# Performance work log

Measured on AMD Instinct MI355X. Metric: run time of the kernel, lower is better.

The kernel has to match this reference:

```python
import jax, jax.numpy as jnp
import numpy as np
import math

IN_CH = 512
KEY_SIZE = 512
VALUE_SIZE = 512
B, T = 8, 2048


def setup_inputs() -> dict:
    key = jax.random.key(0)
    ks = jax.random.split(key, 7)
    s = 1.0 / math.sqrt(IN_CH)
    return {
        "x": jax.random.normal(ks[0], (B, T, IN_CH), dtype=jnp.float32),
        "Wq": jax.random.uniform(ks[1], (IN_CH, KEY_SIZE), jnp.float32, -s, s),
        "bq": jax.random.uniform(ks[2], (KEY_SIZE,), jnp.float32, -s, s),
        "Wk": jax.random.uniform(ks[3], (IN_CH, KEY_SIZE), jnp.float32, -s, s),
        "bk": jax.random.uniform(ks[4], (KEY_SIZE,), jnp.float32, -s, s),
        "Wv": jax.random.uniform(ks[5], (IN_CH, VALUE_SIZE), jnp.float32, -s, s),
        "bv": jax.random.uniform(ks[6], (VALUE_SIZE,), jnp.float32, -s, s),
    }


def reference(x, Wq, bq, Wk, bk, Wv, bv):
    # Projections (single head)
    q = jnp.einsum('btc,ck->btk', x, Wq) + bq  # [B,T,K]
    k = jnp.einsum('btc,ck->btk', x, Wk) + bk  # [B,T,K]
    v = jnp.einsum('btc,cv->btv', x, Wv) + bv  # [B,T,V]
    # Full score matrix, causal mask (strictly upper triangle masked: col > row)
    scores = jnp.einsum('bqk,btk->bqt', q, k)  # [B,T,T]
    t = scores.shape[1]
    causal = jnp.arange(t)[None, :] > jnp.arange(t)[:, None]  # True where future
    scores = jnp.where(causal[None], -jnp.inf, scores)
    attn = jax.nn.softmax(scores / math.sqrt(KEY_SIZE), axis=2)
    out = jnp.einsum('bqt,btv->bqv', attn, v)  # [B,T,V]
    return jnp.concatenate((x, out), axis=2)  # [B,T,C+V]
```

## Files before the change

kernel.cpp:

```cpp
#include <hip/hip_runtime.h>


#define DEV __device__ __forceinline__

typedef unsigned short u16;
typedef unsigned int u32;
typedef __attribute__((ext_vector_type(8))) short short8;
typedef __attribute__((ext_vector_type(4))) float float4v;

DEV u16 f2bf(float f) {
    u32 u = __float_as_uint(f);
    return (u16)((u + 0x7FFFu + ((u >> 16) & 1u)) >> 16);
}
DEV float bf2f(u16 h) { return __uint_as_float(((u32)h) << 16); }

DEV float4v mfma16(short8 a, short8 b, float4v c) {
    return __builtin_amdgcn_mfma_f32_16x16x32_bf16(a, b, c, 0, 0, 0);
}

#define GLD16(gptr, lptr)                                                     \
    __builtin_amdgcn_global_load_lds(                                         \
        (const __attribute__((address_space(1))) void*)(gptr),                \
        (__attribute__((address_space(3))) void*)(lptr), 16, 0, 0)

__global__ void prep_k(const void* __restrict__ x,
                       const void* __restrict__ Wq, const void* __restrict__ Wk,
                       const void* __restrict__ Wv, const void* __restrict__ bq,
                       const void* __restrict__ bk, const void* __restrict__ bv,
                       int* __restrict__ flag, u16* __restrict__ xb,
                       void* __restrict__ out, u16* __restrict__ Wt,
                       u16* __restrict__ bbuf) {
    __shared__ __attribute__((aligned(16))) u16 T[64 * 80];
    int tid = threadIdx.x;
    int lane = tid & 63;
    u32 ws = ((const u32*)x)[lane * 16];
    int e = (ws >> 7) & 0xFF;
    unsigned long long m = __ballot(e >= 0x60 && e <= 0x90);
    int isbf = (__popcll(m) > 32) ? 1 : 0;

    int bid = blockIdx.x;
    if (bid == 0 && tid == 0) flag[0] = isbf;

    if (bid < 4096) {
        int i0 = (bid * 256 + tid) * 8;
        int row = i0 >> 9, col = i0 & 511;
        if (isbf) {
            uint4 v = *(const uint4*)((const u16*)x + i0);
            *(uint4*)&xb[i0] = v;
            *(uint4*)((u16*)out + (size_t)row * 1024 + col) = v;
        } else {
            const float* xf = (const float*)x;
            float4 f0 = *(const float4*)(xf + i0);
            float4 f1 = *(const float4*)(xf + i0 + 4);
            union { u16 us[8]; uint4 v; } pk;
            pk.us[0] = f2bf(f0.x); pk.us[1] = f2bf(f0.y);
            pk.us[2] = f2bf(f0.z); pk.us[3] = f2bf(f0.w);
            pk.us[4] = f2bf(f1.x); pk.us[5] = f2bf(f1.y);
            pk.us[6] = f2bf(f1.z); pk.us[7] = f2bf(f1.w);
            *(uint4*)&xb[i0] = pk.v;
            float* o = (float*)out + (size_t)row * 1024 + col;
            *(float4*)o = f0; *(float4*)(o + 4) = f1;
        }
        return;
    }

    if (bid >= 4288) {
        int j = bid - 4288;
        int z = j >> 1;
        int i = (j & 1) * 256 + tid;
        const void* s = (z == 0) ? bq : ((z == 1) ? bk : bv);
        bbuf[z * 512 + i] = isbf ? ((const u16*)s)[i]
                                 : f2bf(((const float*)s)[i]);
        return;
    }

    int widx = bid - 4096;
    int z = widx >> 6;
    int t64 = widx & 63;
    int k0 = (t64 >> 3) * 64, n0 = (t64 & 7) * 64;
    const void* W = (z == 0) ? Wq : ((z == 1) ? Wk : Wv);
    if (isbf) {
        #pragma unroll
        for (int p = 0; p < 2; p++) {
            int idx = p * 256 + tid;
            int k = idx >> 3, c8 = idx & 7;
            short8 v = *(const short8*)((const u16*)W + (size_t)(k0 + k) * 512 + n0 + c8 * 8);
            #pragma unroll
            for (int j = 0; j < 8; j++)
                T[(c8 * 8 + j) * 80 + k] = (u16)v[j];
        }
    } else {
        #pragma unroll
        for (int p = 0; p < 4; p++) {
            int idx = p * 256 + tid;
            int k = idx >> 4, c4 = idx & 15;
            float4 f = *(const float4*)((const float*)W + (size_t)(k0 + k) * 512 + n0 + c4 * 4);
            T[(c4 * 4 + 0) * 80 + k] = f2bf(f.x);
            T[(c4 * 4 + 1) * 80 + k] = f2bf(f.y);
            T[(c4 * 4 + 2) * 80 + k] = f2bf(f.z);
            T[(c4 * 4 + 3) * 80 + k] = f2bf(f.w);
        }
    }
    __syncthreads();
    #pragma unroll
    for (int p = 0; p < 2; p++) {
        int idx = p * 256 + tid;
        int n = idx >> 3, c8 = idx & 7;
        short8 o = *(const short8*)&T[n * 80 + c8 * 8];
        *(uint4*)&Wt[z * 262144 + (size_t)(n0 + n) * 512 + k0 + c8 * 8] = *(uint4*)&o;
    }
}

#define PWB(N)                                                                \
    do {                                                                      \
        asm volatile("s_waitcnt vmcnt(" #N ")" ::: "memory");                 \
        __builtin_amdgcn_s_barrier();                                         \
        asm volatile("" ::: "memory");                                        \
    } while (0)

__global__ __launch_bounds__(256) void proj_k(
        const u16* __restrict__ x, const u16* __restrict__ Wt,
        const u16* __restrict__ bb,
        u16* __restrict__ Qo, u16* __restrict__ Ko, u16* __restrict__ Vt_out) {
    int L = blockIdx.x;
    int xcd = L & 7;
    int t8 = L >> 3;
    int q8 = t8 / 12;
    int zn = t8 - q8 * 12;
    int mBase = (q8 * 8 + xcd) * 128;
    int z = zn >> 2;
    int nBase = (zn & 3) * 128;
    const u16* Wz = Wt + z * 262144;
    const u16* bias = bb + z * 512;

    __shared__ __attribute__((aligned(16))) u16 LDSBUF[16384];
#define XSB(bi) (&LDSBUF[(bi) * 4096])
#define WSB(bi) (&LDSBUF[8192 + (bi) * 4096])

    int tid = threadIdx.x;
    int w = tid >> 6, lane = tid & 63, quad = lane >> 4, l16 = lane & 15;
    int wr = (w >> 1) * 64, wc = (w & 1) * 64;

#define PISSUE(bi, k0)                                                        \
    { _Pragma("unroll")                                                       \
      for (int gg = 0; gg < 2; gg++) {                                        \
        int g = w * 2 + gg;                                                   \
        int row = g * 16 + (lane >> 2);                                       \
        int c8 = (lane & 3) ^ ((row >> 1) & 3);                               \
        GLD16(&x [(size_t)(mBase + row) * 512 + (k0) + c8 * 8], &XSB(bi)[g * 512]); \
        GLD16(&Wz[(size_t)(nBase + row) * 512 + (k0) + c8 * 8], &WSB(bi)[g * 512]); \
      } }

    PISSUE(0, 0)
    PISSUE(1, 32)

    float4v acc[4][4] = {};

    #pragma unroll 2
    for (int t = 0; t < 16; t++) {
        int bi = t & 1;
        if (t < 15) { PWB(4); } else { PWB(0); }

        short8 a[4], b[4];
        #pragma unroll
        for (int mt = 0; mt < 4; mt++) {
            int rr = wr + mt * 16 + l16;
            a[mt] = *(const short8*)&XSB(bi)[rr * 32 + ((quad ^ ((rr >> 1) & 3)) * 8)];
        }
        #pragma unroll
        for (int nt = 0; nt < 4; nt++) {
            int rr = wc + nt * 16 + l16;
            b[nt] = *(const short8*)&WSB(bi)[rr * 32 + ((quad ^ ((rr >> 1) & 3)) * 8)];
        }
        #pragma unroll
        for (int mt = 0; mt < 4; mt++)
            #pragma unroll
            for (int nt = 0; nt < 4; nt++)
                acc[mt][nt] = mfma16(a[mt], b[nt], acc[mt][nt]);

        if (t < 14) {
            asm volatile("s_waitcnt lgkmcnt(0)" ::: "memory");
            __builtin_amdgcn_s_barrier();
            asm volatile("" ::: "memory");
            PISSUE(bi, (t + 2) * 32)
        }
    }

    __syncthreads();
    u16* stg = &LDSBUF[w * 4096];

    if (z == 2) {
        #pragma unroll
        for (int nt = 0; nt < 4; nt++) {
            int rl = nt * 16 + l16;
            float bval = bf2f(bias[nBase + wc + rl]);
            int rx = rl & 7;
            #pragma unroll
            for (int mt = 0; mt < 4; mt++) {
                int g  = mt * 2 + (quad >> 1);
                int b0 = (quad & 1) * 4;
                float4v v = acc[mt][nt];
                u16 t0 = f2bf(v[0] + bval), t1 = f2bf(v[1] + bval);
                u16 t2 = f2bf(v[2] + bval), t3 = f2bf(v[3] + bval);
                uint2 pk = make_uint2((u32)t0 | ((u32)t1 << 16),
                                      (u32)t2 | ((u32)t3 << 16));
                *(uint2*)&stg[rl * 64 + ((g ^ rx) << 3) + b0] = pk;
            }
        }
        asm volatile("s_waitcnt lgkmcnt(0)" ::: "memory");
        __syncthreads();
        int bbi = (mBase + wr) >> 11;
        int tt0 = (mBase + wr) & 2047;
        #pragma unroll
        for (int i = 0; i < 8; i++) {
            int rl = i * 8 + (lane >> 3);
            int c8 = lane & 7;
            short8 s = *(const short8*)&stg[rl * 64 + ((c8 ^ (rl & 7)) << 3)];
            *(uint4*)&Vt_out[((size_t)bbi * 512 + nBase + wc + rl) * 2048 +
                             tt0 + c8 * 8] = *(uint4*)&s;
        }
    } else {
        u16* dst = (z == 0) ? Qo : Ko;
        #pragma unroll
        for (int nt = 0; nt < 4; nt++) {
            int cl = nt * 16 + l16;
            float bval = bf2f(bias[nBase + wc + cl]);
            int g = nt * 2 + (l16 >> 3);
            int b = l16 & 7;
            #pragma unroll
            for (int mt = 0; mt < 4; mt++) {
                float4v v = acc[mt][nt];
                #pragma unroll
                for (int r = 0; r < 4; r++) {
                    int rl = mt * 16 + quad * 4 + r;
                    stg[rl * 64 + ((g ^ (rl & 7)) << 3) + b] = f2bf(v[r] + bval);
                }
            }
        }
        asm volatile("s_waitcnt lgkmcnt(0)" ::: "memory");
        __syncthreads();
        #pragma unroll
        for (int i = 0; i < 8; i++) {
            int rl = i * 8 + (lane >> 3);
            int c8 = lane & 7;
            short8 s = *(const short8*)&stg[rl * 64 + ((c8 ^ (rl & 7)) << 3)];
            *(uint4*)&dst[(size_t)(mBase + wr + rl) * 512 +
                          nBase + wc + c8 * 8] = *(uint4*)&s;
        }
    }
#undef PISSUE
#undef XSB
#undef WSB
}


#define LOADK(dst, kB, half)                                                  \
    { _Pragma("unroll")                                                       \
      for (int j = 0; j < 8; j++) {                                           \
        int row2 = 2 * (j * 4 + w);                                           \
        int row = row2 + (lane >> 5);                                         \
        int col8 = lane & 31;                                                 \
        GLD16(&Kb[(size_t)((kB) + row) * 512 + (half) * 256 +                 \
                  ((col8 ^ (row & 7)) << 3)], &dst[row2 * 256]);              \
      } }

#define LOADV(dst, kB, half)                                                  \
    { _Pragma("unroll")                                                       \
      for (int j = 0; j < 8; j++) {                                           \
        int blk8 = 8 * (j * 4 + w);                                           \
        int dl = blk8 + (lane >> 3);                                          \
        int col8 = lane & 7;                                                  \
        GLD16(&Vb[(size_t)((half) * 256 + dl) * 2048 + (kB) +                 \
                  ((col8 ^ (dl & 7)) << 3)], &dst[blk8 * 64]);                \
      } }

#define SSTEP(buf, h)                                                         \
    { _Pragma("unroll")                                                       \
      for (int kk = 0; kk < 8; kk++) {                                        \
        _Pragma("unroll")                                                     \
        for (int nt = 0; nt < 4; nt++) {                                      \
          short8 bf = *(const short8*)&buf[(nt * 16 + l16) * 256 +            \
                                           (((kk * 4 + quad) ^ sw) << 3)];    \
          accS[nt] = mfma16(qf[(h) * 8 + kk], bf, accS[nt]);                  \
        } } }

#define PVSTEP(buf, accO)                                                     \
    { _Pragma("unroll")                                                       \
      for (int kk = 0; kk < 2; kk++) {                                        \
        _Pragma("unroll")                                                     \
        for (int dt = 0; dt < 4; dt++) {                                      \
          int rowv = w * 64 + dt * 16 + l16;                                  \
          short8 bf = *(const short8*)&buf[rowv * 64 +                        \
                                           (((kk * 4 + quad) ^ sw) << 3)];    \
          _Pragma("unroll")                                                   \
          for (int mt = 0; mt < 4; mt++)                                      \
            accO[dt][mt] = mfma16(pf[mt][kk], bf, accO[dt][mt]);              \
        } } }

__global__ __launch_bounds__(256, 1) void attn_k(
        const u16* __restrict__ Q, const u16* __restrict__ K,
        const u16* __restrict__ Vt, const int* __restrict__ flag,
        void* __restrict__ out, u16* __restrict__ Opart,
        float2* __restrict__ ml, int dosplit) {
    int blk = blockIdx.x;
    int b, qt, h, kt0, kt1;
    if (dosplit) {
        qt = (blk < 256) ? (31 - (blk >> 4)) : ((blk - 256) >> 4);
        h  = (blk >> 3) & 1;
        b  = blk & 7;
        int n = qt + 1, mid = n >> 1;
        kt0 = h ? mid : 0;
        kt1 = h ? n : mid;
    } else {
        qt = 31 - (blk >> 3);
        h  = 0;
        b  = blk & 7;
        kt0 = 0; kt1 = qt + 1;
    }
    int q0 = qt * 64;
    int isbf = flag[0];

    __shared__ __attribute__((aligned(16))) u16 KV0[16384];
    __shared__ __attribute__((aligned(16))) u16 KV1[16384];
    __shared__ __attribute__((aligned(16))) u16 Ps[4096];
    __shared__ float al_s[64];
    __shared__ float il_s[64];
    __shared__ int skip_s[4];

    int tid = threadIdx.x;
    int w = tid >> 6, lane = tid & 63, quad = lane >> 4, l16 = lane & 15;
    int sw = l16 & 7;

    const u16* Qb = Q  + (size_t)b * 2048 * 512;
    const u16* Kb = K  + (size_t)b * 2048 * 512;
    const u16* Vb = Vt + (size_t)b * 512 * 2048;

    if (kt0 < kt1) LOADK(KV0, kt0 * 64, 0);

    short8 qf[16];
    {
        const u16* Qrow = &Qb[(size_t)(q0 + w * 16 + l16) * 512];
        #pragma unroll
        for (int g = 0; g < 16; g++)
            qf[g] = *(const short8*)&Qrow[g * 32 + quad * 8];
    }

    float4v accO0[4][4] = {};
    float4v accO1[4][4] = {};
    float4v accS[4] = {};
    short8 pf[4][2];
    float mrow[4] = {-1e30f, -1e30f, -1e30f, -1e30f};
    float lrow[4] = {0.f, 0.f, 0.f, 0.f};
    const float scale = 0.044194173824159216f;

    __syncthreads();

    for (int kt = kt0; kt < kt1; kt++) {
        int kB = kt * 64;

        LOADK(KV1, kB, 1);
        SSTEP(KV0, 0);
        __syncthreads();

        LOADV(KV0, kB, 0);
        SSTEP(KV1, 1);
        {
            int diag = (kt == qt);
            float pv[4][4], lmx[4], alpha[4];
            #pragma unroll
            for (int r = 0; r < 4; r++) {
                float mx = -1e30f;
                #pragma unroll
                for (int nt = 0; nt < 4; nt++) {
                    float sv = accS[nt][r] * scale;
                    if (diag && (nt * 16 + l16 > w * 16 + quad * 4 + r)) sv = -1e30f;
                    pv[nt][r] = sv;
                    mx = fmaxf(mx, sv);
                }
                lmx[r] = mx;
            }
            int small = (lmx[0] - mrow[0] <= 8.f) && (lmx[1] - mrow[1] <= 8.f) &&
                        (lmx[2] - mrow[2] <= 8.f) && (lmx[3] - mrow[3] <= 8.f);
            int wskip = __all(small) ? 1 : 0;
            if (lane == 0) skip_s[w] = wskip;
            if (wskip) {
                #pragma unroll
                for (int r = 0; r < 4; r++) alpha[r] = 1.0f;
            } else {
                #pragma unroll
                for (int r = 0; r < 4; r++) {
                    float mx = lmx[r];
                    mx = fmaxf(mx, __shfl_xor(mx, 1));
                    mx = fmaxf(mx, __shfl_xor(mx, 2));
                    mx = fmaxf(mx, __shfl_xor(mx, 4));
                    mx = fmaxf(mx, __shfl_xor(mx, 8));
                    float mnew = fmaxf(mrow[r], mx);
                    alpha[r] = __expf(mrow[r] - mnew);
                    mrow[r] = mnew;
                }
            }
            #pragma unroll
            for (int r = 0; r < 4; r++) {
                float sum = 0.f;
                #pragma unroll
                for (int nt = 0; nt < 4; nt++) {
                    pv[nt][r] = __expf(pv[nt][r] - mrow[r]);
                    sum += pv[nt][r];
                }
                lrow[r] = lrow[r] * alpha[r] + sum;
            }
            #pragma unroll
            for (int nt = 0; nt < 4; nt++)
                #pragma unroll
                for (int r = 0; r < 4; r++)
                    Ps[(w * 16 + quad * 4 + r) * 64 + nt * 16 + l16] = f2bf(pv[nt][r]);
            #pragma unroll
            for (int r = 0; r < 4; r++) al_s[w * 16 + quad * 4 + r] = alpha[r];
            #pragma unroll
            for (int nt = 0; nt < 4; nt++) accS[nt] = (float4v){0.f, 0.f, 0.f, 0.f};
        }
        __syncthreads();

        LOADV(KV1, kB, 1);
        {
            #pragma unroll
            for (int mt = 0; mt < 4; mt++)
                #pragma unroll
                for (int kk = 0; kk < 2; kk++)
                    pf[mt][kk] = *(const short8*)&Ps[(mt * 16 + l16) * 64 +
                                                     kk * 32 + quad * 8];
            int bskip = skip_s[0] & skip_s[1] & skip_s[2] & skip_s[3];
            if (!bskip) {
                float alf[4][4];
                #pragma unroll
                for (int mt = 0; mt < 4; mt++)
                    #pragma unroll
                    for (int r = 0; r < 4; r++)
                        alf[mt][r] = al_s[mt * 16 + quad * 4 + r];
                #pragma unroll
                for (int dt = 0; dt < 4; dt++)
                    #pragma unroll
                    for (int mt = 0; mt < 4; mt++)
                        #pragma unroll
                        for (int r = 0; r < 4; r++) {
                            accO0[dt][mt][r] *= alf[mt][r];
                            accO1[dt][mt][r] *= alf[mt][r];
                        }
            }
        }
        PVSTEP(KV0, accO0);
        __syncthreads();

        if (kt + 1 < kt1) LOADK(KV0, kB + 64, 0);
        PVSTEP(KV1, accO1);
        __syncthreads();
    }

    #pragma unroll
    for (int r = 0; r < 4; r++) {
        lrow[r] += __shfl_xor(lrow[r], 1);
        lrow[r] += __shfl_xor(lrow[r], 2);
        lrow[r] += __shfl_xor(lrow[r], 4);
        lrow[r] += __shfl_xor(lrow[r], 8);
    }

    if (dosplit) {
        if (l16 == 0) {
            #pragma unroll
            for (int r = 0; r < 4; r++) {
                int grow = b * 2048 + q0 + w * 16 + quad * 4 + r;
                ml[h * 16384 + grow] = make_float2(mrow[r], lrow[r]);
            }
        }
        #pragma unroll
        for (int dt = 0; dt < 4; dt++) {
            int dg = w * 64 + dt * 16 + l16;
            #pragma unroll
            for (int mt = 0; mt < 4; mt++)
                #pragma unroll
                for (int r = 0; r < 4; r++) {
                    int grow = b * 2048 + q0 + mt * 16 + quad * 4 + r;
                    size_t base = ((size_t)h * 16384 + grow) * 512;
                    Opart[base + dg]       = f2bf(accO0[dt][mt][r]);
                    Opart[base + dg + 256] = f2bf(accO1[dt][mt][r]);
                }
        }
    } else {
        #pragma unroll
        for (int r = 0; r < 4; r++) il_s[w * 16 + quad * 4 + r] = 1.0f / lrow[r];
        __syncthreads();
        float invl[4][4];
        #pragma unroll
        for (int mt = 0; mt < 4; mt++)
            #pragma unroll
            for (int r = 0; r < 4; r++) invl[mt][r] = il_s[mt * 16 + quad * 4 + r];
        u16*   o16 = (u16*)out;
        float* o32 = (float*)out;
        #pragma unroll
        for (int dt = 0; dt < 4; dt++) {
            int dg0 = 512 + w * 64 + dt * 16 + l16;
            #pragma unroll
            for (int mt = 0; mt < 4; mt++)
                #pragma unroll
                for (int r = 0; r < 4; r++) {
                    int rowg = q0 + mt * 16 + quad * 4 + r;
                    size_t base = ((size_t)b * 2048 + rowg) * 1024;
                    float v0 = accO0[dt][mt][r] * invl[mt][r];
                    float v1 = accO1[dt][mt][r] * invl[mt][r];
                    if (isbf) {
                        o16[base + dg0]       = f2bf(v0);
                        o16[base + dg0 + 256] = f2bf(v1);
                    } else {
                        o32[base + dg0]       = v0;
                        o32[base + dg0 + 256] = v1;
                    }
                }
        }
    }
}

__global__ __launch_bounds__(256) void combine_k(
        const u16* __restrict__ Opart, const float2* __restrict__ ml,
        const int* __restrict__ flag, void* __restrict__ out) {
    int tid = threadIdx.x;
    int grow = blockIdx.x * 4 + (tid >> 6);
    int d0 = (tid & 63) * 8;
    float2 ml0 = ml[grow], ml1 = ml[16384 + grow];
    float m = fmaxf(ml0.x, ml1.x);
    float a0 = __expf(ml0.x - m), a1 = __expf(ml1.x - m);
    float il = 1.0f / (ml0.y * a0 + ml1.y * a1);
    a0 *= il; a1 *= il;
    uint4 v0 = *(const uint4*)&Opart[(size_t)grow * 512 + d0];
    uint4 v1 = *(const uint4*)&Opart[(size_t)(16384 + grow) * 512 + d0];
    const u16* u0 = (const u16*)&v0;
    const u16* u1 = (const u16*)&v1;
    float res[8];
    #pragma unroll
    for (int i = 0; i < 8; i++)
        res[i] = bf2f(u0[i]) * a0 + bf2f(u1[i]) * a1;
    size_t base = (size_t)grow * 1024 + 512 + d0;
    if (flag[0]) {
        union { u16 us[8]; uint4 v; } pk;
        #pragma unroll
        for (int i = 0; i < 8; i++) pk.us[i] = f2bf(res[i]);
        *(uint4*)((u16*)out + base) = pk.v;
    } else {
        float* o = (float*)out + base;
        *(float4*)o = make_float4(res[0], res[1], res[2], res[3]);
        *(float4*)(o + 4) = make_float4(res[4], res[5], res[6], res[7]);
    }
}

extern "C" void kernel_launch(void* const* d_in, const int* in_sizes, int n_in,
                              void* d_out, int out_size, void* d_ws, size_t ws_size,
                              hipStream_t stream) {
    const void* x  = d_in[0];
    const void* Wq = d_in[1];
    const void* bq = d_in[2];
    const void* Wk = d_in[3];
    const void* bk = d_in[4];
    const void* Wv = d_in[5];
    const void* bv = d_in[6];

    u16* base = (u16*)d_ws;
    int* flag = (int*)base;
    u16* Wt   = base + 8;
    u16* bb   = Wt + 786432;
    u16* xb   = bb + 1544;
    u16* Qw   = xb + 8388608;
    u16* Kw   = Qw + 8388608;
    u16* Vtw  = Kw + 8388608;
    u16* Opart = Vtw + 8388608;
    float2* mlb = (float2*)(Opart + 16777216);

    size_t need = ((size_t)(Opart - base) + 16777216) * 2 + 262144;
    int dosplit = (ws_size >= need) ? 1 : 0;

    hipLaunchKernelGGL(prep_k, dim3(4294), dim3(256), 0, stream,
                       x, Wq, Wk, Wv, bq, bk, bv, flag, xb, d_out, Wt, bb);
    hipLaunchKernelGGL(proj_k, dim3(1536), dim3(256), 0, stream, xb, Wt, bb, Qw, Kw, Vtw);
    if (dosplit) {
        hipLaunchKernelGGL(attn_k, dim3(512), dim3(256), 0, stream,
                           Qw, Kw, Vtw, flag, d_out, Opart, mlb, 1);
        hipLaunchKernelGGL(combine_k, dim3(4096), dim3(256), 0, stream,
                           Opart, mlb, flag, d_out);
    } else {
        hipLaunchKernelGGL(attn_k, dim3(256), dim3(256), 0, stream,
                           Qw, Kw, Vtw, flag, d_out, Opart, mlb, 0);
    }
}
```

Before: 255.4 us.

## Fuse split-K combine into attention kernel via per-tile atomic counter

Removes the separate combine kernel. Each split attention block increments a per-(qtile,batch) counter after writing its partial output and softmax stats, and the second block to finish merges both halves and writes the final output. The counter is zeroed in the prep kernel. This saves a kernel launch and lets the merge overlap with other blocks' work, at the cost of threadfences, an atomic, and a serialized combine tail in the last-finishing block.

```diff
diff --git a/kernel.cpp b/kernel.cpp
--- a/kernel.cpp
+++ b/kernel.cpp
@@ -29,7 +29,7 @@
                        const void* __restrict__ bk, const void* __restrict__ bv,
                        int* __restrict__ flag, u16* __restrict__ xb,
                        void* __restrict__ out, u16* __restrict__ Wt,
-                       u16* __restrict__ bbuf) {
+                       u16* __restrict__ bbuf, int* __restrict__ cnt) {
     __shared__ __attribute__((aligned(16))) u16 T[64 * 80];
     int tid = threadIdx.x;
     int lane = tid & 63;
@@ -66,6 +66,7 @@
 
     if (bid >= 4288) {
         int j = bid - 4288;
+        if (j == 0) cnt[tid] = 0;
         int z = j >> 1;
         int i = (j & 1) * 256 + tid;
         const void* s = (z == 0) ? bq : ((z == 1) ? bk : bv);
@@ -301,7 +302,7 @@
         const u16* __restrict__ Q, const u16* __restrict__ K,
         const u16* __restrict__ Vt, const int* __restrict__ flag,
         void* __restrict__ out, u16* __restrict__ Opart,
-        float2* __restrict__ ml, int dosplit) {
+        float2* __restrict__ ml, int* __restrict__ cnt, int dosplit) {
     int blk = blockIdx.x;
     int b, qt, h, kt0, kt1;
     if (dosplit) {
@@ -326,6 +327,7 @@
     __shared__ float al_s[64];
     __shared__ float il_s[64];
     __shared__ int skip_s[4];
+    __shared__ int comb_s;
 
     int tid = threadIdx.x;
     int w = tid >> 6, lane = tid & 63, quad = lane >> 4, l16 = lane & 15;
@@ -484,6 +486,48 @@
                     Opart[base + dg]       = f2bf(accO0[dt][mt][r]);
                     Opart[base + dg + 256] = f2bf(accO1[dt][mt][r]);
                 }
+        }
+
+        __threadfence();
+        __syncthreads();
+        if (tid == 0) {
+            int old = atomicAdd(&cnt[qt * 8 + b], 1);
+            comb_s = (old == 1);
+        }
+        __syncthreads();
+        if (comb_s) {
+            __threadfence();
+            u16*   o16 = (u16*)out;
+            float* o32 = (float*)out;
+            #pragma unroll 4
+            for (int it = 0; it < 16; it++) {
+                int grow = b * 2048 + q0 + it * 4 + (tid >> 6);
+                int d0 = (tid & 63) * 8;
+                float2 ml0 = ml[grow], ml1 = ml[16384 + grow];
+                float mm = fmaxf(ml0.x, ml1.x);
+                float a0 = __expf(ml0.x - mm), a1 = __expf(ml1.x - mm);
+                float il = 1.0f / (ml0.y * a0 + ml1.y * a1);
+                a0 *= il; a1 *= il;
+                uint4 v0 = *(const uint4*)&Opart[(size_t)grow * 512 + d0];
+                uint4 v1 = *(const uint4*)&Opart[(size_t)(16384 + grow) * 512 + d0];
+                const u16* u0 = (const u16*)&v0;
+                const u16* u1 = (const u16*)&v1;
+                float res[8];
+                #pragma unroll
+                for (int i = 0; i < 8; i++)
+                    res[i] = bf2f(u0[i]) * a0 + bf2f(u1[i]) * a1;
+                size_t base = (size_t)grow * 1024 + 512 + d0;
+                if (isbf) {
+                    union { u16 us[8]; uint4 v; } pk;
+                    #pragma unroll
+                    for (int i = 0; i < 8; i++) pk.us[i] = f2bf(res[i]);
+                    *(uint4*)(o16 + base) = pk.v;
+                } else {
+                    float* o = o32 + base;
+                    *(float4*)o = make_float4(res[0], res[1], res[2], res[3]);
+                    *(float4*)(o + 4) = make_float4(res[4], res[5], res[6], res[7]);
+                }
+            }
         }
     } else {
         #pragma unroll
@@ -519,38 +563,6 @@
     }
 }
 
-__global__ __launch_bounds__(256) void combine_k(
-        const u16* __restrict__ Opart, const float2* __restrict__ ml,
-        const int* __restrict__ flag, void* __restrict__ out) {
-    int tid = threadIdx.x;
-    int grow = blockIdx.x * 4 + (tid >> 6);
-    int d0 = (tid & 63) * 8;
-    float2 ml0 = ml[grow], ml1 = ml[16384 + grow];
-    float m = fmaxf(ml0.x, ml1.x);
-    float a0 = __expf(ml0.x - m), a1 = __expf(ml1.x - m);
-    float il = 1.0f / (ml0.y * a0 + ml1.y * a1);
-    a0 *= il; a1 *= il;
-    uint4 v0 = *(const uint4*)&Opart[(size_t)grow * 512 + d0];
-    uint4 v1 = *(const uint4*)&Opart[(size_t)(16384 + grow) * 512 + d0];
-    const u16* u0 = (const u16*)&v0;
-    const u16* u1 = (const u16*)&v1;
-    float res[8];
-    #pragma unroll
-    for (int i = 0; i < 8; i++)
-        res[i] = bf2f(u0[i]) * a0 + bf2f(u1[i]) * a1;
-    size_t base = (size_t)grow * 1024 + 512 + d0;
-    if (flag[0]) {
-        union { u16 us[8]; uint4 v; } pk;
-        #pragma unroll
-        for (int i = 0; i < 8; i++) pk.us[i] = f2bf(res[i]);
-        *(uint4*)((u16*)out + base) = pk.v;
-    } else {
-        float* o = (float*)out + base;
-        *(float4*)o = make_float4(res[0], res[1], res[2], res[3]);
-        *(float4*)(o + 4) = make_float4(res[4], res[5], res[6], res[7]);
-    }
-}
-
 extern "C" void kernel_launch(void* const* d_in, const int* in_sizes, int n_in,
                               void* d_out, int out_size, void* d_ws, size_t ws_size,
                               hipStream_t stream) {
@@ -572,20 +584,19 @@
     u16* Vtw  = Kw + 8388608;
     u16* Opart = Vtw + 8388608;
     float2* mlb = (float2*)(Opart + 16777216);
-
-    size_t need = ((size_t)(Opart - base) + 16777216) * 2 + 262144;
+    int* cnt = (int*)(mlb + 32768);
+
+    size_t need = ((size_t)(Opart - base) + 16777216) * 2 + 262144 + 1024;
     int dosplit = (ws_size >= need) ? 1 : 0;
 
     hipLaunchKernelGGL(prep_k, dim3(4294), dim3(256), 0, stream,
-                       x, Wq, Wk, Wv, bq, bk, bv, flag, xb, d_out, Wt, bb);
+                       x, Wq, Wk, Wv, bq, bk, bv, flag, xb, d_out, Wt, bb, cnt);
     hipLaunchKernelGGL(proj_k, dim3(1536), dim3(256), 0, stream, xb, Wt, bb, Qw, Kw, Vtw);
     if (dosplit) {
         hipLaunchKernelGGL(attn_k, dim3(512), dim3(256), 0, stream,
-                           Qw, Kw, Vtw, flag, d_out, Opart, mlb, 1);
-        hipLaunchKernelGGL(combine_k, dim3(4096), dim3(256), 0, stream,
-                           Opart, mlb, flag, d_out);
+                           Qw, Kw, Vtw, flag, d_out, Opart, mlb, cnt, 1);
     } else {
         hipLaunchKernelGGL(attn_k, dim3(256), dim3(256), 0, stream,
-                           Qw, Kw, Vtw, flag, d_out, Opart, mlb, 0);
+                           Qw, Kw, Vtw, flag, d_out, Opart, mlb, cnt, 0);
     }
 }
```

Result: slower. 419.0 us (+64.0%).
